# Optimization experiments

Hardware: AMD Instinct MI355X
Metric: run time of the kernel (lower is better)

The kernel has to match this reference:

```python
import jax, jax.numpy as jnp
import numpy as np

ALPHA = 0.1

def setup_inputs() -> dict:
    key = jax.random.key(0)
    x = jax.random.normal(key, (64, 8192, 64), dtype=jnp.float32)
    return {"x": x}

def reference(x):
    # EMA recurrence along axis -2: y_0 = x_0, y_t = alpha*x_t + (1-alpha)*y_{t-1}
    alpha = jnp.asarray(ALPHA, x.dtype)
    one_m = jnp.asarray(1.0 - ALPHA, x.dtype)
    xt = jnp.moveaxis(x, -2, 0)  # [T, B, F]

    def step(carry, xcur):
        y = alpha * xcur + one_m * carry
        return y, y

    y0 = xt[0]
    _, ys = jax.lax.scan(step, y0, xt[1:])
    out = jnp.concatenate([y0[None], ys], axis=0)  # [T, B, F]
    return jnp.moveaxis(out, 0, -2)
```

## Files before the change

### kernel.cpp

```cpp
#include <hip/hip_runtime.h>


constexpr int Tn = 8192;
constexpr int Fn = 64;
constexpr int Ln = 128;
constexpr int Hn = 64;
constexpr int PF = 32;
constexpr float ALPHA = 0.1f;
constexpr float OMA   = 0.9f;

__global__ __launch_bounds__(256) void ema_kernel(const float* __restrict__ x,
                                                  float* __restrict__ y) {
    const int f  = threadIdx.x & 63;
    const int sL = threadIdx.x >> 6;
    const int b  = blockIdx.x >> 4;
    const int c  = ((blockIdx.x & 15) << 2) | sL;

    const size_t base = (size_t)b * (Tn * Fn) + f;
    const float* __restrict__ xp = x + base;
    float*       __restrict__ yp = y + base;

    const int t0 = c * Ln;
    float s;
    float buf[PF];
    int t, nblk;

    if (c != 0) {
        s = 0.0f;
        t = t0 - Hn;
        for (int blk = 0; blk < Hn / PF; ++blk) {
            #pragma unroll
            for (int i = 0; i < PF; ++i) buf[i] = xp[(size_t)(t + i) * Fn];
            #pragma unroll
            for (int i = 0; i < PF; ++i) s = fmaf(OMA, s, ALPHA * buf[i]);
            t += PF;
        }
        nblk = Ln / PF;
    } else {
        #pragma unroll
        for (int i = 0; i < PF; ++i) buf[i] = xp[(size_t)i * Fn];
        s = buf[0];
        __builtin_nontemporal_store(s, &yp[0]);
        #pragma unroll
        for (int i = 1; i < PF; ++i) {
            s = fmaf(OMA, s, ALPHA * buf[i]);
            __builtin_nontemporal_store(s, &yp[(size_t)i * Fn]);
        }
        t = PF;
        nblk = Ln / PF - 1;
    }

    for (int blk = 0; blk < nblk; ++blk) {
        #pragma unroll
        for (int i = 0; i < PF; ++i) buf[i] = xp[(size_t)(t + i) * Fn];
        #pragma unroll
        for (int i = 0; i < PF; ++i) {
            s = fmaf(OMA, s, ALPHA * buf[i]);
            __builtin_nontemporal_store(s, &yp[(size_t)(t + i) * Fn]);
        }
        t += PF;
    }
}

extern "C" void kernel_launch(void* const* d_in, const int* in_sizes, int n_in,
                              void* d_out, int out_size, void* d_ws, size_t ws_size,
                              hipStream_t stream) {
    const float* x = (const float*)d_in[0];
    float*       y = (float*)d_out;
    ema_kernel<<<dim3(1024), dim3(256), 0, stream>>>(x, y);
}
```

Before: 231.9 us.

## Stage input through LDS with 128-bit loads and double-buffered register prefetch

Each wave now loads 16-timestep tiles with float4 global loads into per-wave LDS buffers, then runs the scalar recurrence from LDS. Register prefetch of the next tile overlaps global latency with the sequential FMA chain. The goal is fewer, wider memory transactions and better latency hiding. In exchange it adds LDS traffic, uses 32 KB of LDS per block, and relies on wave-synchronous LDS use with no barriers.

```diff
diff --git a/kernel.cpp b/kernel.cpp
--- a/kernel.cpp
+++ b/kernel.cpp
@@ -1,64 +1,86 @@
 #include <hip/hip_runtime.h>
 
+
+typedef float fx4 __attribute__((ext_vector_type(4)));
 
 constexpr int Tn = 8192;
 constexpr int Fn = 64;
 constexpr int Ln = 128;
 constexpr int Hn = 64;
-constexpr int PF = 32;
+constexpr int PF = 16;
 constexpr float ALPHA = 0.1f;
 constexpr float OMA   = 0.9f;
 
 __global__ __launch_bounds__(256) void ema_kernel(const float* __restrict__ x,
                                                   float* __restrict__ y) {
-    const int f  = threadIdx.x & 63;
-    const int sL = threadIdx.x >> 6;
-    const int b  = blockIdx.x >> 4;
-    const int c  = ((blockIdx.x & 15) << 2) | sL;
+    const int lane = threadIdx.x & 63;
+    const int w    = threadIdx.x >> 6;
+    const int b    = blockIdx.x >> 4;
+    const int c    = ((blockIdx.x & 15) << 2) | w;
 
-    const size_t base = (size_t)b * (Tn * Fn) + f;
-    const float* __restrict__ xp = x + base;
-    float*       __restrict__ yp = y + base;
+    const size_t bb = (size_t)b * (Tn * Fn);
+    const float* __restrict__ xp = x + bb;
+    float*       __restrict__ yp = y + bb;
 
-    const int t0 = c * Ln;
-    float s;
-    float buf[PF];
-    int t, nblk;
+    __shared__ float lds[4][2][PF * Fn];
+    float (* __restrict__ Lb)[PF * Fn] = lds[w];
 
-    if (c != 0) {
-        s = 0.0f;
-        t = t0 - Hn;
-        for (int blk = 0; blk < Hn / PF; ++blk) {
-            #pragma unroll
-            for (int i = 0; i < PF; ++i) buf[i] = xp[(size_t)(t + i) * Fn];
-            #pragma unroll
-            for (int i = 0; i < PF; ++i) s = fmaf(OMA, s, ALPHA * buf[i]);
-            t += PF;
+    const int lr = lane >> 4;
+    const int lf = (lane & 15) << 2;
+
+    const int tstart = (c == 0) ? 0 : c * Ln - Hn;
+    const int nb     = (c == 0) ? Ln / PF : (Ln + Hn) / PF;
+    const int sb     = (c == 0) ? 0 : Hn / PF;
+
+    auto LOADG = [&](int t0, fx4& g0, fx4& g1, fx4& g2, fx4& g3) {
+        const float* p = xp + (size_t)(t0 + lr) * Fn + lf;
+        g0 = *(const fx4*)(p);
+        g1 = *(const fx4*)(p + 4 * Fn);
+        g2 = *(const fx4*)(p + 8 * Fn);
+        g3 = *(const fx4*)(p + 12 * Fn);
+    };
+    auto WRITE = [&](float* buf, fx4 g0, fx4 g1, fx4 g2, fx4 g3) {
+        float* q = buf + lr * Fn + lf;
+        *(fx4*)(q)          = g0;
+        *(fx4*)(q + 4 * Fn) = g1;
+        *(fx4*)(q + 8 * Fn) = g2;
+        *(fx4*)(q + 12 * Fn) = g3;
+    };
+    float s = 0.0f;
+    auto CONSUME = [&](const float* buf, int bt, bool dostore, bool first) {
+        int i0 = 0;
+        if (first) {
+            s = buf[lane];
+            __builtin_nontemporal_store(s, &yp[(size_t)bt * Fn + lane]);
+            i0 = 1;
         }
-        nblk = Ln / PF;
-    } else {
-        #pragma unroll
-        for (int i = 0; i < PF; ++i) buf[i] = xp[(size_t)i * Fn];
-        s = buf[0];
-        __builtin_nontemporal_store(s, &yp[0]);
-        #pragma unroll
-        for (int i = 1; i < PF; ++i) {
-            s = fmaf(OMA, s, ALPHA * buf[i]);
-            __builtin_nontemporal_store(s, &yp[(size_t)i * Fn]);
-        }
-        t = PF;
-        nblk = Ln / PF - 1;
-    }
-
-    for (int blk = 0; blk < nblk; ++blk) {
-        #pragma unroll
-        for (int i = 0; i < PF; ++i) buf[i] = xp[(size_t)(t + i) * Fn];
         #pragma unroll
         for (int i = 0; i < PF; ++i) {
-            s = fmaf(OMA, s, ALPHA * buf[i]);
-            __builtin_nontemporal_store(s, &yp[(size_t)(t + i) * Fn]);
+            if (i < i0) continue;
+            s = fmaf(OMA, s, ALPHA * buf[i * Fn + lane]);
+            if (dostore)
+                __builtin_nontemporal_store(s, &yp[(size_t)(bt + i) * Fn + lane]);
         }
-        t += PF;
+    };
+
+    fx4 a0, a1, a2, a3, b0, b1, b2, b3;
+
+    LOADG(tstart, a0, a1, a2, a3);
+    WRITE(Lb[0], a0, a1, a2, a3);
+    LOADG(tstart + PF, b0, b1, b2, b3);
+
+    int k = 0;
+    while (true) {
+        CONSUME(Lb[0], tstart + k * PF, k >= sb, (c == 0) && (k == 0));
+        if (k + 1 >= nb) break;
+        WRITE(Lb[1], b0, b1, b2, b3);
+        if (k + 2 < nb) LOADG(tstart + (k + 2) * PF, a0, a1, a2, a3);
+        ++k;
+        CONSUME(Lb[1], tstart + k * PF, k >= sb, false);
+        if (k + 1 >= nb) break;
+        WRITE(Lb[0], a0, a1, a2, a3);
+        if (k + 2 < nb) LOADG(tstart + (k + 2) * PF, b0, b1, b2, b3);
+        ++k;
     }
 }
 
```

Measured after the change: 239.5 us. 3.3% more time.

## Stage chunk loads through LDS with async global_load_lds and smaller chunks

Applied to the files above, without the earlier changes.

Each single-wave workgroup now takes a 64-step chunk plus a 64-step warmup halo. It issues all loads up front as 16-byte async global-to-LDS copies, then waits on vmcnt so the halo warmup can start before the rest of the chunk arrives. The grid grows to 8192 workgroups with a swizzled block-to-chunk mapping. The goal is more memory-level parallelism and wider loads, in exchange for a larger redundant halo read (now equal to the chunk length) and a reliance on hand-written waitcnt ordering.

```diff
diff --git a/kernel.cpp b/kernel.cpp
--- a/kernel.cpp
+++ b/kernel.cpp
@@ -3,62 +3,73 @@
 
 constexpr int Tn = 8192;
 constexpr int Fn = 64;
-constexpr int Ln = 128;
+constexpr int Ln = 64;
 constexpr int Hn = 64;
-constexpr int PF = 32;
+constexpr int NC = Tn / Ln;
 constexpr float ALPHA = 0.1f;
 constexpr float OMA   = 0.9f;
 
-__global__ __launch_bounds__(256) void ema_kernel(const float* __restrict__ x,
-                                                  float* __restrict__ y) {
-    const int f  = threadIdx.x & 63;
-    const int sL = threadIdx.x >> 6;
-    const int b  = blockIdx.x >> 4;
-    const int c  = ((blockIdx.x & 15) << 2) | sL;
+#define AS_GLOBAL __attribute__((address_space(1)))
+#define AS_LDS    __attribute__((address_space(3)))
 
-    const size_t base = (size_t)b * (Tn * Fn) + f;
-    const float* __restrict__ xp = x + base;
-    float*       __restrict__ yp = y + base;
+__global__ __launch_bounds__(64) void ema_kernel(const float* __restrict__ x,
+                                                 float* __restrict__ y) {
+    __shared__ __align__(16) float tile[(Hn + Ln) * Fn];
+
+    const int lane = threadIdx.x;
+    const int wg = ((blockIdx.x & 7) << 10) | (blockIdx.x >> 3);
+    const int b  = wg >> 7;
+    const int c  = wg & (NC - 1);
+
+    const size_t bb = (size_t)b * (Tn * Fn);
+    const float* __restrict__ xp = x + bb;
+    float*       __restrict__ yp = y + bb;
+
+    const int lr = lane >> 4;
+    const int lf = (lane & 15) << 2;
 
     const int t0 = c * Ln;
+    const int tstart = (c == 0) ? 0 : t0 - Hn;
+
     float s;
-    float buf[PF];
-    int t, nblk;
-
     if (c != 0) {
+        #pragma unroll
+        for (int j = 0; j < (Hn + Ln) / 4; ++j) {
+            const float* g = xp + (size_t)(tstart + 4 * j + lr) * Fn + lf;
+            __builtin_amdgcn_global_load_lds(
+                (const AS_GLOBAL float*)g,
+                (AS_LDS float*)&tile[j * (4 * Fn)], 16, 0, 0);
+        }
+        asm volatile("s_waitcnt vmcnt(16)" ::: "memory");
+        __builtin_amdgcn_sched_barrier(0);
         s = 0.0f;
-        t = t0 - Hn;
-        for (int blk = 0; blk < Hn / PF; ++blk) {
-            #pragma unroll
-            for (int i = 0; i < PF; ++i) buf[i] = xp[(size_t)(t + i) * Fn];
-            #pragma unroll
-            for (int i = 0; i < PF; ++i) s = fmaf(OMA, s, ALPHA * buf[i]);
-            t += PF;
+        #pragma unroll
+        for (int i = 0; i < Hn; ++i)
+            s = fmaf(OMA, s, ALPHA * tile[i * Fn + lane]);
+        asm volatile("s_waitcnt vmcnt(0)" ::: "memory");
+        __builtin_amdgcn_sched_barrier(0);
+        #pragma unroll
+        for (int i = 0; i < Ln; ++i) {
+            s = fmaf(OMA, s, ALPHA * tile[(Hn + i) * Fn + lane]);
+            __builtin_nontemporal_store(s, &yp[(size_t)(t0 + i) * Fn + lane]);
         }
-        nblk = Ln / PF;
     } else {
         #pragma unroll
-        for (int i = 0; i < PF; ++i) buf[i] = xp[(size_t)i * Fn];
-        s = buf[0];
-        __builtin_nontemporal_store(s, &yp[0]);
+        for (int j = 0; j < Ln / 4; ++j) {
+            const float* g = xp + (size_t)(4 * j + lr) * Fn + lf;
+            __builtin_amdgcn_global_load_lds(
+                (const AS_GLOBAL float*)g,
+                (AS_LDS float*)&tile[j * (4 * Fn)], 16, 0, 0);
+        }
+        asm volatile("s_waitcnt vmcnt(0)" ::: "memory");
+        __builtin_amdgcn_sched_barrier(0);
+        s = tile[lane];
+        __builtin_nontemporal_store(s, &yp[lane]);
         #pragma unroll
-        for (int i = 1; i < PF; ++i) {
-            s = fmaf(OMA, s, ALPHA * buf[i]);
-            __builtin_nontemporal_store(s, &yp[(size_t)i * Fn]);
+        for (int i = 1; i < Ln; ++i) {
+            s = fmaf(OMA, s, ALPHA * tile[i * Fn + lane]);
+            __builtin_nontemporal_store(s, &yp[(size_t)i * Fn + lane]);
         }
-        t = PF;
-        nblk = Ln / PF - 1;
-    }
-
-    for (int blk = 0; blk < nblk; ++blk) {
-        #pragma unroll
-        for (int i = 0; i < PF; ++i) buf[i] = xp[(size_t)(t + i) * Fn];
-        #pragma unroll
-        for (int i = 0; i < PF; ++i) {
-            s = fmaf(OMA, s, ALPHA * buf[i]);
-            __builtin_nontemporal_store(s, &yp[(size_t)(t + i) * Fn]);
-        }
-        t += PF;
     }
 }
 
@@ -67,5 +78,5 @@
                               hipStream_t stream) {
     const float* x = (const float*)d_in[0];
     float*       y = (float*)d_out;
-    ema_kernel<<<dim3(1024), dim3(256), 0, stream>>>(x, y);
+    ema_kernel<<<dim3(8192), dim3(64), 0, stream>>>(x, y);
 }
```

New measurement: 233.4 us. No clear change (+0.6%).

## Halve EMA chunk length and hand-pipeline loads with inline asm and vmcnt waits

Applied to the files above, without the earlier changes.

Each wave now computes a 64-step chunk instead of 128, still after a 64-step warm-up. That doubles the number of independent recurrence chains, at the cost of re-reading more input. Loads and stores are issued as inline-asm global_load/store_dword into four rotating 8-register buffers, with explicit s_waitcnt vmcnt thresholds so memory latency overlaps the serial FMA chain. Blocks grow to 512 threads, use a block-index swizzle, and drop the nontemporal stores.

```diff
diff --git a/kernel.cpp b/kernel.cpp
--- a/kernel.cpp
+++ b/kernel.cpp
@@ -3,62 +3,106 @@
 
 constexpr int Tn = 8192;
 constexpr int Fn = 64;
-constexpr int Ln = 128;
+constexpr int Ln = 64;
 constexpr int Hn = 64;
-constexpr int PF = 32;
+constexpr int NC = Tn / Ln;
 constexpr float ALPHA = 0.1f;
 constexpr float OMA   = 0.9f;
 
-__global__ __launch_bounds__(256) void ema_kernel(const float* __restrict__ x,
-                                                  float* __restrict__ y) {
-    const int f  = threadIdx.x & 63;
-    const int sL = threadIdx.x >> 6;
-    const int b  = blockIdx.x >> 4;
-    const int c  = ((blockIdx.x & 15) << 2) | sL;
+#define WAITV(N) do { asm volatile("s_waitcnt vmcnt(" #N ")" ::: "memory"); \
+                      __builtin_amdgcn_sched_barrier(0); } while (0)
 
-    const size_t base = (size_t)b * (Tn * Fn) + f;
-    const float* __restrict__ xp = x + base;
-    float*       __restrict__ yp = y + base;
+#define LD1(dst, p, BOFF) \
+  asm volatile("global_load_dword %0, %1, off offset:" #BOFF \
+               : "=v"(dst) : "v"(p) : "memory")
 
+#define ST1(p, val, BOFF) \
+  asm volatile("global_store_dword %0, %1, off offset:" #BOFF \
+               :: "v"(p), "v"(val) : "memory")
+
+#define LD8(R, p) do { \
+  LD1(R[0], (p), 0);    LD1(R[1], (p), 256);  LD1(R[2], (p), 512);  \
+  LD1(R[3], (p), 768);  LD1(R[4], (p), 1024); LD1(R[5], (p), 1280); \
+  LD1(R[6], (p), 1536); LD1(R[7], (p), 1792); } while (0)
+
+#define C8(R) do { \
+  s = fmaf(OMA, s, ALPHA * R[0]); s = fmaf(OMA, s, ALPHA * R[1]); \
+  s = fmaf(OMA, s, ALPHA * R[2]); s = fmaf(OMA, s, ALPHA * R[3]); \
+  s = fmaf(OMA, s, ALPHA * R[4]); s = fmaf(OMA, s, ALPHA * R[5]); \
+  s = fmaf(OMA, s, ALPHA * R[6]); s = fmaf(OMA, s, ALPHA * R[7]); } while (0)
+
+#define C8S(R, q) do { \
+  s = fmaf(OMA, s, ALPHA * R[0]); ST1((q), s, 0);    \
+  s = fmaf(OMA, s, ALPHA * R[1]); ST1((q), s, 256);  \
+  s = fmaf(OMA, s, ALPHA * R[2]); ST1((q), s, 512);  \
+  s = fmaf(OMA, s, ALPHA * R[3]); ST1((q), s, 768);  \
+  s = fmaf(OMA, s, ALPHA * R[4]); ST1((q), s, 1024); \
+  s = fmaf(OMA, s, ALPHA * R[5]); ST1((q), s, 1280); \
+  s = fmaf(OMA, s, ALPHA * R[6]); ST1((q), s, 1536); \
+  s = fmaf(OMA, s, ALPHA * R[7]); ST1((q), s, 1792); } while (0)
+
+#define C8S0(R, q) do { \
+  s = R[0];                       ST1((q), s, 0);    \
+  s = fmaf(OMA, s, ALPHA * R[1]); ST1((q), s, 256);  \
+  s = fmaf(OMA, s, ALPHA * R[2]); ST1((q), s, 512);  \
+  s = fmaf(OMA, s, ALPHA * R[3]); ST1((q), s, 768);  \
+  s = fmaf(OMA, s, ALPHA * R[4]); ST1((q), s, 1024); \
+  s = fmaf(OMA, s, ALPHA * R[5]); ST1((q), s, 1280); \
+  s = fmaf(OMA, s, ALPHA * R[6]); ST1((q), s, 1536); \
+  s = fmaf(OMA, s, ALPHA * R[7]); ST1((q), s, 1792); } while (0)
+
+__global__ __launch_bounds__(512, 8) void ema_kernel(const float* __restrict__ x,
+                                                     float* __restrict__ y) {
+    const int lane = threadIdx.x & 63;
+    const int swz = ((blockIdx.x & 7) << 7) | (blockIdx.x >> 3);
+    const int G   = (swz << 3) | (threadIdx.x >> 6);
+    const int b   = G >> 7;
+    const int c   = G & (NC - 1);
+
+    const size_t bb = (size_t)b * (Tn * Fn);
     const int t0 = c * Ln;
-    float s;
-    float buf[PF];
-    int t, nblk;
+    const int tstart = (c == 0) ? 0 : t0 - Hn;
+
+    const float* px = x + bb + (size_t)tstart * Fn + lane;
+    float*       py = y + bb + (size_t)t0 * Fn + lane;
+
+    float rA[8], rB[8], rC[8], rD[8];
+    float s = 0.0f;
 
     if (c != 0) {
-        s = 0.0f;
-        t = t0 - Hn;
-        for (int blk = 0; blk < Hn / PF; ++blk) {
-            #pragma unroll
-            for (int i = 0; i < PF; ++i) buf[i] = xp[(size_t)(t + i) * Fn];
-            #pragma unroll
-            for (int i = 0; i < PF; ++i) s = fmaf(OMA, s, ALPHA * buf[i]);
-            t += PF;
-        }
-        nblk = Ln / PF;
+        LD8(rA, px + 0 * 512);
+        LD8(rB, px + 1 * 512);
+        LD8(rC, px + 2 * 512);
+        LD8(rD, px + 3 * 512);
+        WAITV(24); C8(rA); LD8(rA, px + 4 * 512);
+        WAITV(24); C8(rB); LD8(rB, px + 5 * 512);
+        WAITV(24); C8(rC); LD8(rC, px + 6 * 512);
+        WAITV(24); C8(rD); LD8(rD, px + 7 * 512);
+        WAITV(24); C8(rA); LD8(rA, px + 8 * 512);
+        WAITV(24); C8(rB); LD8(rB, px + 9 * 512);
+        WAITV(24); C8(rC); LD8(rC, px + 10 * 512);
+        WAITV(24); C8(rD); LD8(rD, px + 11 * 512);
+        WAITV(24); C8S(rA, py + 0 * 512); LD8(rA, px + 12 * 512);
+        WAITV(32); C8S(rB, py + 1 * 512); LD8(rB, px + 13 * 512);
+        WAITV(40); C8S(rC, py + 2 * 512); LD8(rC, px + 14 * 512);
+        WAITV(48); C8S(rD, py + 3 * 512); LD8(rD, px + 15 * 512);
+        WAITV(48); C8S(rA, py + 4 * 512);
+        WAITV(40); C8S(rB, py + 5 * 512);
+        WAITV(32); C8S(rC, py + 6 * 512);
+        WAITV(24); C8S(rD, py + 7 * 512);
     } else {
-        #pragma unroll
-        for (int i = 0; i < PF; ++i) buf[i] = xp[(size_t)i * Fn];
-        s = buf[0];
-        __builtin_nontemporal_store(s, &yp[0]);
-        #pragma unroll
-        for (int i = 1; i < PF; ++i) {
-            s = fmaf(OMA, s, ALPHA * buf[i]);
-            __builtin_nontemporal_store(s, &yp[(size_t)i * Fn]);
-        }
-        t = PF;
-        nblk = Ln / PF - 1;
-    }
-
-    for (int blk = 0; blk < nblk; ++blk) {
-        #pragma unroll
-        for (int i = 0; i < PF; ++i) buf[i] = xp[(size_t)(t + i) * Fn];
-        #pragma unroll
-        for (int i = 0; i < PF; ++i) {
-            s = fmaf(OMA, s, ALPHA * buf[i]);
-            __builtin_nontemporal_store(s, &yp[(size_t)(t + i) * Fn]);
-        }
-        t += PF;
+        LD8(rA, px + 0 * 512);
+        LD8(rB, px + 1 * 512);
+        LD8(rC, px + 2 * 512);
+        LD8(rD, px + 3 * 512);
+        WAITV(24); C8S0(rA, py + 0 * 512); LD8(rA, px + 4 * 512);
+        WAITV(32); C8S(rB, py + 1 * 512);  LD8(rB, px + 5 * 512);
+        WAITV(40); C8S(rC, py + 2 * 512);  LD8(rC, px + 6 * 512);
+        WAITV(48); C8S(rD, py + 3 * 512);  LD8(rD, px + 7 * 512);
+        WAITV(48); C8S(rA, py + 4 * 512);
+        WAITV(40); C8S(rB, py + 5 * 512);
+        WAITV(32); C8S(rC, py + 6 * 512);
+        WAITV(24); C8S(rD, py + 7 * 512);
     }
 }
 
@@ -67,5 +111,5 @@
                               hipStream_t stream) {
     const float* x = (const float*)d_in[0];
     float*       y = (float*)d_out;
-    ema_kernel<<<dim3(1024), dim3(256), 0, stream>>>(x, y);
+    ema_kernel<<<dim3(1024), dim3(512), 0, stream>>>(x, y);
 }
```

After: 237.8 us. +2.5%, slower.
